# Kernel tuning notes

Measured on AMD Instinct MI355X. Metric: run time of the kernel, lower is better.

Reference implementation:

```python
import jax, jax.numpy as jnp
import numpy as np

DEPTH = 6
NB_CLASSES = 10
INPUT_SIZE = 4096
N_INTERNAL = 2**DEPTH - 1  # 63
N_LEAVES = 2**DEPTH       # 64
T = 8192


def setup_inputs() -> dict:
    key = jax.random.key(0)
    k1, k2, k3, k4, k5 = jax.random.split(key, 5)
    input_traj = jax.random.normal(k1, (T, INPUT_SIZE), dtype=jnp.float32)
    # node gates: Linear(input_size, 1) per internal node, stacked [N, D]
    W = jax.random.normal(k2, (N_INTERNAL, INPUT_SIZE), dtype=jnp.float32) / np.sqrt(INPUT_SIZE)
    b = jax.random.normal(k3, (N_INTERNAL,), dtype=jnp.float32) * 0.01
    beta = jax.random.uniform(k4, (N_INTERNAL,), dtype=jnp.float32)  # torch.rand(1) per node
    leaf_dist = jax.random.uniform(k5, (N_LEAVES, NB_CLASSES), dtype=jnp.float32)
    class_reward = jnp.arange(NB_CLASSES, dtype=jnp.float32)
    return {"input_traj": input_traj, "W": W, "b": b, "beta": beta,
            "leaf_dist": leaf_dist, "class_reward": class_reward}


def reference(input_traj, W, b, beta, leaf_dist, class_reward):
    # Node gating probs for all T states and all internal nodes at once.
    # Original: sigmoid(beta * fc(x)) per node, per state. [T, N_INTERNAL]
    P = jax.nn.sigmoid(beta[None, :] * (input_traj @ W.T + b[None, :]))
    # Path probabilities down the complete binary tree (BFS/heap layout:
    # level k occupies node indices [2^k - 1, 2^(k+1) - 1)). child[0] gets p,
    # child[1] gets (1 - p).
    t = input_traj.shape[0]
    pp = jnp.ones((t, 1), dtype=P.dtype)
    offset = 0
    for k in range(DEPTH):
        n = 1 << k
        Pl = P[:, offset:offset + n]            # [T, n]
        pp = jnp.stack([pp * Pl, pp * (1.0 - Pl)], axis=-1).reshape(t, 2 * n)
        offset += n
    # pp: [T, N_LEAVES], leaves in left-to-right order.
    # Leaf reward: inner(class_reward, softmax(distribution)) per leaf. [L]
    leaf_r = jnp.sum(jax.nn.softmax(leaf_dist, axis=-1) * class_reward[None, :], axis=-1)
    # Trajectory reward: sum over states and leaves of path_prob * leaf reward.
    return jnp.sum(pp @ leaf_r)
```

## Files before the change

### kernel.cpp

```cpp
#include <hip/hip_runtime.h>
#include <hip/hip_bf16.h>

#define T_ROWS   8192
#define K_DIM    4096
#define N_INT    63
#define N_LEAF   64
#define NCLS     10

typedef __bf16 bf16x8 __attribute__((ext_vector_type(8)));
typedef __bf16 bf16x4 __attribute__((ext_vector_type(4)));
typedef float  f32x4  __attribute__((ext_vector_type(4)));

__global__ __launch_bounds__(256) void sdt_prep(
    const float* __restrict__ W,
    const float* __restrict__ leaf_dist,
    const float* __restrict__ class_reward,
    __bf16* __restrict__ Wb,
    float* __restrict__ leaf_r,
    float* __restrict__ out)
{
    int gid  = blockIdx.x * 256 + threadIdx.x;
    int base = gid * 4;
    int n    = base >> 12;
    bf16x4 v;
    if (n < N_INT) {
        const float4 w = *reinterpret_cast<const float4*>(W + base);
        v[0] = (__bf16)w.x; v[1] = (__bf16)w.y; v[2] = (__bf16)w.z; v[3] = (__bf16)w.w;
    } else {
        v[0] = (__bf16)0.0f; v[1] = (__bf16)0.0f; v[2] = (__bf16)0.0f; v[3] = (__bf16)0.0f;
    }
    *reinterpret_cast<bf16x4*>(Wb + base) = v;

    if (blockIdx.x == 0) {
        if (threadIdx.x < N_LEAF) {
            int i = threadIdx.x;
            float m = -1e30f;
            #pragma unroll
            for (int j = 0; j < NCLS; ++j) m = fmaxf(m, leaf_dist[i * NCLS + j]);
            float s = 0.0f, d = 0.0f;
            #pragma unroll
            for (int j = 0; j < NCLS; ++j) {
                float e = expf(leaf_dist[i * NCLS + j] - m);
                s += e;
                d += e * class_reward[j];
            }
            leaf_r[i] = d / s;
        } else if (threadIdx.x == N_LEAF) {
            out[0] = 0.0f;
        }
    }
}

__global__ __launch_bounds__(256, 4) void sdt_main(
    const float* __restrict__ X,
    const __bf16* __restrict__ Wb,
    const float* __restrict__ b,
    const float* __restrict__ beta,
    const float* __restrict__ leaf_r,
    float* __restrict__ out)
{
    __shared__ float red[4 * 16 * 65];
    __shared__ float Pbuf[16 * 64];
    __shared__ float sred[4];

    const int tid  = threadIdx.x;
    const int wid  = tid >> 6;
    const int lane = tid & 63;
    const int m16  = lane & 15;
    const int q    = lane >> 4;

    const int row0 = blockIdx.x * 16;
    const int kbase = wid * (K_DIM / 4);

    const f32x4* Ap = reinterpret_cast<const f32x4*>(
        X + (size_t)(row0 + m16) * K_DIM + kbase + q * 8);
    const __bf16* B0 = Wb + (size_t)(0 * 16 + m16) * K_DIM + kbase + q * 8;
    const __bf16* B1 = Wb + (size_t)(1 * 16 + m16) * K_DIM + kbase + q * 8;
    const __bf16* B2 = Wb + (size_t)(2 * 16 + m16) * K_DIM + kbase + q * 8;
    const __bf16* B3 = Wb + (size_t)(3 * 16 + m16) * K_DIM + kbase + q * 8;

    f32x4 acc[4];
    #pragma unroll
    for (int g = 0; g < 4; ++g) acc[g] = (f32x4){0.0f, 0.0f, 0.0f, 0.0f};

    f32x4 c0 = __builtin_nontemporal_load(Ap);
    f32x4 c1 = __builtin_nontemporal_load(Ap + 1);

    #pragma unroll 2
    for (int it = 0; it < 32; ++it) {
        f32x4 n0, n1;
        if (it < 31) {
            n0 = __builtin_nontemporal_load(Ap + (it + 1) * 8);
            n1 = __builtin_nontemporal_load(Ap + (it + 1) * 8 + 1);
        }
        bf16x8 af;
        af[0] = (__bf16)c0[0]; af[1] = (__bf16)c0[1];
        af[2] = (__bf16)c0[2]; af[3] = (__bf16)c0[3];
        af[4] = (__bf16)c1[0]; af[5] = (__bf16)c1[1];
        af[6] = (__bf16)c1[2]; af[7] = (__bf16)c1[3];
        const int ko = it * 32;
        const bf16x8 bf0 = *reinterpret_cast<const bf16x8*>(B0 + ko);
        const bf16x8 bf1 = *reinterpret_cast<const bf16x8*>(B1 + ko);
        const bf16x8 bf2 = *reinterpret_cast<const bf16x8*>(B2 + ko);
        const bf16x8 bf3 = *reinterpret_cast<const bf16x8*>(B3 + ko);
        acc[0] = __builtin_amdgcn_mfma_f32_16x16x32_bf16(af, bf0, acc[0], 0, 0, 0);
        acc[1] = __builtin_amdgcn_mfma_f32_16x16x32_bf16(af, bf1, acc[1], 0, 0, 0);
        acc[2] = __builtin_amdgcn_mfma_f32_16x16x32_bf16(af, bf2, acc[2], 0, 0, 0);
        acc[3] = __builtin_amdgcn_mfma_f32_16x16x32_bf16(af, bf3, acc[3], 0, 0, 0);
        c0 = n0; c1 = n1;
    }

    #pragma unroll
    for (int g = 0; g < 4; ++g)
        #pragma unroll
        for (int r = 0; r < 4; ++r)
            red[(wid * 16 + q * 4 + r) * 65 + g * 16 + m16] = acc[g][r];
    __syncthreads();

    for (int e = tid; e < 16 * 64; e += 256) {
        const int r = e >> 6, c = e & 63;
        float s = 0.0f;
        #pragma unroll
        for (int w = 0; w < 4; ++w) s += red[(w * 16 + r) * 65 + c];
        float P = 0.0f;
        if (c < N_INT) {
            const float z = beta[c] * (s + b[c]);
            P = 1.0f / (1.0f + __expf(-z));
        }
        Pbuf[r * 64 + c] = P;
    }
    __syncthreads();

    const int row = tid >> 4;
    const int t16 = tid & 15;
    float score = 0.0f;
    #pragma unroll
    for (int u = 0; u < 4; ++u) {
        const int leaf = t16 * 4 + u;
        float prod = 1.0f;
        #pragma unroll
        for (int k = 0; k < 6; ++k) {
            const int node = ((1 << k) - 1) + (leaf >> (6 - k));
            const float p  = Pbuf[row * 64 + node];
            const int bit  = (leaf >> (5 - k)) & 1;
            prod *= bit ? (1.0f - p) : p;
        }
        score += prod * leaf_r[leaf];
    }

    #pragma unroll
    for (int off = 32; off > 0; off >>= 1)
        score += __shfl_down(score, off, 64);
    if (lane == 0) sred[wid] = score;
    __syncthreads();
    if (tid == 0) {
        float s = sred[0] + sred[1] + sred[2] + sred[3];
        atomicAdd(out, s);
    }
}

extern "C" void kernel_launch(void* const* d_in, const int* in_sizes, int n_in,
                              void* d_out, int out_size, void* d_ws, size_t ws_size,
                              hipStream_t stream)
{
    const float* X           = (const float*)d_in[0];
    const float* W           = (const float*)d_in[1];
    const float* b           = (const float*)d_in[2];
    const float* beta        = (const float*)d_in[3];
    const float* leaf_dist   = (const float*)d_in[4];
    const float* class_rew   = (const float*)d_in[5];
    float* out               = (float*)d_out;

    __bf16* Wb    = (__bf16*)d_ws;
    float*  leafr = (float*)((char*)d_ws + (size_t)N_LEAF * K_DIM * 2);

    sdt_prep<<<256, 256, 0, stream>>>(W, leaf_dist, class_rew, Wb, leafr, out);
    sdt_main<<<T_ROWS / 16, 256, 0, stream>>>(X, Wb, b, beta, leafr, out);
}
```

Before: 226.7 us.

## Stage X chunks into LDS via async global_load_lds with double buffering

Replaces each lane's strided direct global loads of X rows with cooperative global-to-LDS DMA loads. Each wave instruction now fetches contiguous 1 KB row segments into a double-buffered 512-column chunk. Waves then read their K-slice from LDS, convert to bf16 and feed MFMA, while the next chunk streams in. The reduction and probability buffers are aliased onto the staging buffer to save LDS. The larger LDS footprint lowers target occupancy from 4 to 2 blocks per CU, and correctness depends on the compiler inserting a wait for the async loads before each barrier.

```diff
diff --git a/kernel.cpp b/kernel.cpp
--- a/kernel.cpp
+++ b/kernel.cpp
@@ -7,9 +7,18 @@
 #define N_LEAF   64
 #define NCLS     10
 
+#define BM       16
+#define CHUNK    512
+#define NCHUNK   (K_DIM / CHUNK)
+#define ASTRIDE  516
+
 typedef __bf16 bf16x8 __attribute__((ext_vector_type(8)));
 typedef __bf16 bf16x4 __attribute__((ext_vector_type(4)));
 typedef float  f32x4  __attribute__((ext_vector_type(4)));
+
+#define GLOAD_LDS16(g, l) __builtin_amdgcn_global_load_lds(              \
+    (const __attribute__((address_space(1))) void*)(g),                  \
+    (__attribute__((address_space(3))) void*)(l), 16, 0, 0)
 
 __global__ __launch_bounds__(256) void sdt_prep(
     const float* __restrict__ W,
@@ -51,7 +60,7 @@
     }
 }
 
-__global__ __launch_bounds__(256, 4) void sdt_main(
+__global__ __launch_bounds__(256, 2) void sdt_main(
     const float* __restrict__ X,
     const __bf16* __restrict__ Wb,
     const float* __restrict__ b,
@@ -59,9 +68,10 @@
     const float* __restrict__ leaf_r,
     float* __restrict__ out)
 {
-    __shared__ float red[4 * 16 * 65];
-    __shared__ float Pbuf[16 * 64];
+    __shared__ float Ash[2 * BM * ASTRIDE];
     __shared__ float sred[4];
+    float* red  = Ash;
+    float* Pbuf = Ash + 4 * 16 * 65;
 
     const int tid  = threadIdx.x;
     const int wid  = tid >> 6;
@@ -69,45 +79,59 @@
     const int m16  = lane & 15;
     const int q    = lane >> 4;
 
-    const int row0 = blockIdx.x * 16;
-    const int kbase = wid * (K_DIM / 4);
-
-    const f32x4* Ap = reinterpret_cast<const f32x4*>(
-        X + (size_t)(row0 + m16) * K_DIM + kbase + q * 8);
-    const __bf16* B0 = Wb + (size_t)(0 * 16 + m16) * K_DIM + kbase + q * 8;
-    const __bf16* B1 = Wb + (size_t)(1 * 16 + m16) * K_DIM + kbase + q * 8;
-    const __bf16* B2 = Wb + (size_t)(2 * 16 + m16) * K_DIM + kbase + q * 8;
-    const __bf16* B3 = Wb + (size_t)(3 * 16 + m16) * K_DIM + kbase + q * 8;
+    const int row0   = blockIdx.x * BM;
+    const int kslice = wid * (CHUNK / 4);
+
+    const __bf16* B0 = Wb + (size_t)(0 * 16 + m16) * K_DIM + kslice + q * 8;
+    const __bf16* B1 = Wb + (size_t)(1 * 16 + m16) * K_DIM + kslice + q * 8;
+    const __bf16* B2 = Wb + (size_t)(2 * 16 + m16) * K_DIM + kslice + q * 8;
+    const __bf16* B3 = Wb + (size_t)(3 * 16 + m16) * K_DIM + kslice + q * 8;
 
     f32x4 acc[4];
     #pragma unroll
     for (int g = 0; g < 4; ++g) acc[g] = (f32x4){0.0f, 0.0f, 0.0f, 0.0f};
 
-    f32x4 c0 = __builtin_nontemporal_load(Ap);
-    f32x4 c1 = __builtin_nontemporal_load(Ap + 1);
-
-    #pragma unroll 2
-    for (int it = 0; it < 32; ++it) {
-        f32x4 n0, n1;
-        if (it < 31) {
-            n0 = __builtin_nontemporal_load(Ap + (it + 1) * 8);
-            n1 = __builtin_nontemporal_load(Ap + (it + 1) * 8 + 1);
-        }
-        bf16x8 af;
-        af[0] = (__bf16)c0[0]; af[1] = (__bf16)c0[1];
-        af[2] = (__bf16)c0[2]; af[3] = (__bf16)c0[3];
-        af[4] = (__bf16)c1[0]; af[5] = (__bf16)c1[1];
-        af[6] = (__bf16)c1[2]; af[7] = (__bf16)c1[3];
-        const int ko = it * 32;
-        const bf16x8 bf0 = *reinterpret_cast<const bf16x8*>(B0 + ko);
-        const bf16x8 bf1 = *reinterpret_cast<const bf16x8*>(B1 + ko);
-        const bf16x8 bf2 = *reinterpret_cast<const bf16x8*>(B2 + ko);
-        const bf16x8 bf3 = *reinterpret_cast<const bf16x8*>(B3 + ko);
-        acc[0] = __builtin_amdgcn_mfma_f32_16x16x32_bf16(af, bf0, acc[0], 0, 0, 0);
-        acc[1] = __builtin_amdgcn_mfma_f32_16x16x32_bf16(af, bf1, acc[1], 0, 0, 0);
-        acc[2] = __builtin_amdgcn_mfma_f32_16x16x32_bf16(af, bf2, acc[2], 0, 0, 0);
-        acc[3] = __builtin_amdgcn_mfma_f32_16x16x32_bf16(af, bf3, acc[3], 0, 0, 0);
-        c0 = n0; c1 = n1;
+    auto stage = [&](int buf, int c) {
+        #pragma unroll
+        for (int i = 0; i < 8; ++i) {
+            const int seg  = wid * 8 + i;
+            const int row  = seg >> 1;
+            const int half = seg & 1;
+            const float* g = X + (size_t)(row0 + row) * K_DIM
+                               + c * CHUNK + half * 256 + lane * 4;
+            float* l = Ash + buf * (BM * ASTRIDE) + row * ASTRIDE + half * 256;
+            GLOAD_LDS16(g, l);
+        }
+    };
+
+    stage(0, 0);
+
+    for (int c = 0; c < NCHUNK; ++c) {
+        __syncthreads();
+        if (c + 1 < NCHUNK) stage((c + 1) & 1, c + 1);
+
+        const float* Ab = Ash + (c & 1) * (BM * ASTRIDE) + (size_t)m16 * ASTRIDE;
+        const int kg = c * CHUNK;
+        #pragma unroll
+        for (int s = 0; s < 4; ++s) {
+            const int kc = kslice + s * 32 + q * 8;
+            const f32x4 a0 = *reinterpret_cast<const f32x4*>(Ab + kc);
+            const f32x4 a1 = *reinterpret_cast<const f32x4*>(Ab + kc + 4);
+            bf16x8 af;
+            af[0] = (__bf16)a0[0]; af[1] = (__bf16)a0[1];
+            af[2] = (__bf16)a0[2]; af[3] = (__bf16)a0[3];
+            af[4] = (__bf16)a1[0]; af[5] = (__bf16)a1[1];
+            af[6] = (__bf16)a1[2]; af[7] = (__bf16)a1[3];
+            const int ko = kg + s * 32;
+            const bf16x8 bf0 = *reinterpret_cast<const bf16x8*>(B0 + ko);
+            const bf16x8 bf1 = *reinterpret_cast<const bf16x8*>(B1 + ko);
+            const bf16x8 bf2 = *reinterpret_cast<const bf16x8*>(B2 + ko);
+            const bf16x8 bf3 = *reinterpret_cast<const bf16x8*>(B3 + ko);
+            acc[0] = __builtin_amdgcn_mfma_f32_16x16x32_bf16(af, bf0, acc[0], 0, 0, 0);
+            acc[1] = __builtin_amdgcn_mfma_f32_16x16x32_bf16(af, bf1, acc[1], 0, 0, 0);
+            acc[2] = __builtin_amdgcn_mfma_f32_16x16x32_bf16(af, bf2, acc[2], 0, 0, 0);
+            acc[3] = __builtin_amdgcn_mfma_f32_16x16x32_bf16(af, bf3, acc[3], 0, 0, 0);
+        }
     }
 
     #pragma unroll
@@ -175,5 +199,5 @@
     float*  leafr = (float*)((char*)d_ws + (size_t)N_LEAF * K_DIM * 2);
 
     sdt_prep<<<256, 256, 0, stream>>>(W, leaf_dist, class_rew, Wb, leafr, out);
-    sdt_main<<<T_ROWS / 16, 256, 0, stream>>>(X, Wb, b, beta, leafr, out);
+    sdt_main<<<T_ROWS / BM, 256, 0, stream>>>(X, Wb, b, beta, leafr, out);
 }
```

Result: faster. 218.8 us (-3.5%).
